# Kernel optimization log

Measured on AMD Instinct MI355X. Metric: run time of the kernel, lower is better.

The kernel has to match this reference:

```python
import jax, jax.numpy as jnp
import numpy as np

B, LENGTH = 4, 65494
FILTS = 256        # sinc out channels == attention seq len == d_model (BN constraint)
KERNEL = 1025      # first_conv=1024 -> forced odd
D_MODEL = 256
N_HEADS = 8
D_FF = 1024
E_LAYERS = 4
C_OUT = 2
IN_SIZE = 21490
SR = 16000


def _to_mel(hz):
    return 2595 * np.log10(1 + hz / 700)


def _to_hz(mel):
    return 700 * (10 ** (mel / 2595) - 1)


def make_sinc_filters():
    out_ch = FILTS + 1
    f = (SR // 2) * np.linspace(0, 1, 257)  # NFFT=512 -> 257 bins
    fmel = _to_mel(f)
    mels = np.linspace(fmel.min(), fmel.max(), out_ch + 2)
    freq = _to_hz(mels)[:out_ch]
    hsupp = np.arange(-(KERNEL - 1) / 2, (KERNEL - 1) / 2 + 1)
    ham = np.hamming(KERNEL)
    bp = np.zeros((FILTS, KERNEL), dtype=np.float32)
    for i in range(FILTS):
        fmin, fmax = freq[i], freq[i + 1]
        h_hi = 2 * fmax / SR * np.sinc(2 * fmax * hsupp / SR)
        h_lo = 2 * fmin / SR * np.sinc(2 * fmin * hsupp / SR)
        bp[i] = (ham * (h_hi - h_lo)).astype(np.float32)
    return jnp.asarray(bp).reshape(FILTS, 1, KERNEL)


def layernorm(x, g, b, eps=1e-5):
    m = x.mean(-1, keepdims=True)
    v = x.var(-1, keepdims=True)
    return (x - m) / jnp.sqrt(v + eps) * g + b


def batchnorm(x, g, b, eps=1e-5):
    # training-mode BatchNorm1d over [B, C, T]: stats over (0, 2)
    m = x.mean((0, 2), keepdims=True)
    v = x.var((0, 2), keepdims=True)
    return (x - m) / jnp.sqrt(v + eps) * g[None, :, None] + b[None, :, None]


def positional(n):
    pos = jnp.arange(n, dtype=jnp.float32)[:, None]
    div = jnp.exp(jnp.arange(0, D_MODEL, 2, dtype=jnp.float32) * (-np.log(10000.0) / D_MODEL))
    pe = jnp.zeros((n, D_MODEL), jnp.float32)
    pe = pe.at[:, 0::2].set(jnp.sin(pos * div)).at[:, 1::2].set(jnp.cos(pos * div))
    return pe


def _forward(x, filters, bn1_g, bn1_b, emb_w, emb_b, embbn_g, embbn_b,
             wq, bq, wk, bk, wv, bv, wo, bo, c1w, c1b, c2w, c2b,
             ln1g, ln1b, ln2g, ln2b, lnfg, lnfb, projw, projb):
    Bb = x.shape[0]
    # SincConv: [B,1,L] -> [B, FILTS, L-K+1]
    h = jax.lax.conv_general_dilated(x[:, None, :], filters, (1,), 'VALID',
                                     dimension_numbers=('NCH', 'OIH', 'NCH'))
    h = jnp.abs(h)
    T = h.shape[-1] // 3
    h = h[..., :T * 3].reshape(Bb, FILTS, T, 3).max(-1)  # max_pool1d(k=3)
    h = jax.nn.selu(batchnorm(h, bn1_g, bn1_b))          # [B, FILTS, 21490]
    # LinearEmbedding: Linear(21490 -> d_model) + BN + ReLU + pos emb
    e = jnp.einsum('bct,dt->bcd', h, emb_w) + emb_b      # [B, FILTS, D_MODEL]
    e = jax.nn.relu(batchnorm(e, embbn_g, embbn_b))
    z = e + positional(e.shape[1])[None]
    hd = D_MODEL // N_HEADS
    scale = 1.0 / np.sqrt(hd)
    for l in range(E_LAYERS):
        q = (z @ wq[l].T + bq[l]).reshape(Bb, FILTS, N_HEADS, hd)
        k = (z @ wk[l].T + bk[l]).reshape(Bb, FILTS, N_HEADS, hd)
        v = (z @ wv[l].T + bv[l]).reshape(Bb, FILTS, N_HEADS, hd)
        scores = jnp.einsum('blhe,bshe->bhls', q, k) * scale  # mask_flag=False
        attn = jax.nn.softmax(scores, axis=-1)
        o = jnp.einsum('bhls,bshd->blhd', attn, v).reshape(Bb, FILTS, D_MODEL)
        o = o @ wo[l].T + bo[l]
        z = layernorm(z + o, ln1g[l], ln1b[l])
        y = jax.nn.gelu(jnp.einsum('bld,fd->blf', z, c1w[l]) + c1b[l], approximate=False)
        y = jnp.einsum('blf,df->bld', y, c2w[l]) + c2b[l]
        z = layernorm(z + y, ln2g[l], ln2b[l])
    z = layernorm(z, lnfg, lnfb)
    pooled = z.mean(axis=1)
    return pooled @ projw.T + projb  # [B, C_OUT]


def setup_inputs() -> dict:
    key = jax.random.key(0)
    ks = jax.random.split(key, 16)
    rn = lambda k, s, sc=0.02: jax.random.normal(k, s, jnp.float32) * sc
    d = {}
    d['x'] = jax.random.normal(ks[0], (B, LENGTH), jnp.float32)
    d['filters'] = make_sinc_filters()
    d['bn1_g'] = jnp.ones((FILTS,), jnp.float32)
    d['bn1_b'] = jnp.zeros((FILTS,), jnp.float32)
    d['emb_w'] = rn(ks[1], (D_MODEL, IN_SIZE))
    d['emb_b'] = jnp.zeros((D_MODEL,), jnp.float32)
    d['embbn_g'] = jnp.ones((D_MODEL,), jnp.float32)
    d['embbn_b'] = jnp.zeros((D_MODEL,), jnp.float32)
    d['wq'] = rn(ks[2], (E_LAYERS, D_MODEL, D_MODEL))
    d['bq'] = jnp.zeros((E_LAYERS, D_MODEL), jnp.float32)
    d['wk'] = rn(ks[3], (E_LAYERS, D_MODEL, D_MODEL))
    d['bk'] = jnp.zeros((E_LAYERS, D_MODEL), jnp.float32)
    d['wv'] = rn(ks[4], (E_LAYERS, D_MODEL, D_MODEL))
    d['bv'] = jnp.zeros((E_LAYERS, D_MODEL), jnp.float32)
    d['wo'] = rn(ks[5], (E_LAYERS, D_MODEL, D_MODEL))
    d['bo'] = jnp.zeros((E_LAYERS, D_MODEL), jnp.float32)
    d['c1w'] = rn(ks[6], (E_LAYERS, D_FF, D_MODEL))
    d['c1b'] = jnp.zeros((E_LAYERS, D_FF), jnp.float32)
    d['c2w'] = rn(ks[7], (E_LAYERS, D_MODEL, D_FF))
    d['c2b'] = jnp.zeros((E_LAYERS, D_MODEL), jnp.float32)
    d['ln1g'] = jnp.ones((E_LAYERS, D_MODEL), jnp.float32)
    d['ln1b'] = jnp.zeros((E_LAYERS, D_MODEL), jnp.float32)
    d['ln2g'] = jnp.ones((E_LAYERS, D_MODEL), jnp.float32)
    d['ln2b'] = jnp.zeros((E_LAYERS, D_MODEL), jnp.float32)
    d['lnfg'] = jnp.ones((D_MODEL,), jnp.float32)
    d['lnfb'] = jnp.zeros((D_MODEL,), jnp.float32)
    d['projw'] = rn(ks[8], (C_OUT, D_MODEL))
    d['projb'] = jnp.zeros((C_OUT,), jnp.float32)
    return d


def reference(x, filters, bn1_g, bn1_b, emb_w, emb_b, embbn_g, embbn_b,
              wq, bq, wk, bk, wv, bv, wo, bo, c1w, c1b, c2w, c2b,
              ln1g, ln1b, ln2g, ln2b, lnfg, lnfb, projw, projb):
    return _forward(x, filters, bn1_g, bn1_b, emb_w, emb_b, embbn_g, embbn_b,
                    wq, bq, wk, bk, wv, bv, wo, bo, c1w, c1b, c2w, c2b,
                    ln1g, ln1b, ln2g, ln2b, lnfg, lnfb, projw, projb)
```

## Files before the change

kernel.cpp:

```cpp
#include <hip/hip_runtime.h>
#include <math.h>

#define L_IN 65494
#define T_POOL 21490
#define TPP 21496
#define KF 1025
#define RS 1144
#define NCH 141
#define KEMB 21490
#define KEMBP 21504
#define NKC 1344
#define FTILE 33280
#define LWSZ 786432

typedef short s16x4 __attribute__((ext_vector_type(4)));
typedef _Float16 f16x8 __attribute__((ext_vector_type(8)));
typedef float f32x4 __attribute__((ext_vector_type(4)));
typedef float f32x16 __attribute__((ext_vector_type(16)));

__device__ inline float selu_f(float x) {
    float e = expf(fminf(x, 0.f));
    float neg = 1.6732632423543772f * (e - 1.f);
    return 1.0507009873554805f * (x > 0.f ? x : neg);
}

__device__ inline float gelu_f(float x) {
    return 0.5f * x * (1.f + erff(x * 0.7071067811865476f));
}

__device__ inline float dot4(float4 a, float4 b) {
    return fmaf(a.x, b.x, fmaf(a.y, b.y, fmaf(a.z, b.z, a.w * b.w)));
}

__device__ inline float sel4(float a0, float a1, float a2, float a3, int i) {
    float r = a0;
    r = (i == 1) ? a1 : r;
    r = (i == 2) ? a2 : r;
    r = (i == 3) ? a3 : r;
    return r;
}

__device__ inline short f2h_bits(float v) {
    _Float16 h = (_Float16)v;
    return *(short*)&h;
}

__device__ inline void f16split(float v, short& hs, short& ls) {
    _Float16 h = (_Float16)v;
    float hf = (float)h;
    _Float16 l = (_Float16)(v - hf);
    hs = *(short*)&h;
    ls = *(short*)&l;
}

__device__ inline void f16split2(float v, _Float16& h, _Float16& l) {
    h = (_Float16)v;
    l = (_Float16)(v - (float)h);
}

__global__ __launch_bounds__(512)
void filt_pack_kernel(const float* __restrict__ filt, short* __restrict__ fpH) {
    int blk = blockIdx.x;
    int ft = blk / 65, kc = blk % 65;
    int t = threadIdx.x, lane = t >> 3, e = t & 7;
    int f = ft * 32 + (lane & 31);
    int tap = kc * 16 + (lane >> 5) * 8 + e;
    float v = (tap < KF) ? filt[f * KF + tap] : 0.f;
    fpH[blk * 512 + t] = f2h_bits(v);
}

__global__ __launch_bounds__(512)
void wpack_kernel(const float* __restrict__ wsrc, short* __restrict__ wpH) {
    int blk = blockIdx.x;
    int ft = blk / NKC, kc = blk % NKC;
    int t = threadIdx.x, lane = t >> 3, e = t & 7;
    int row = ft * 32 + (lane & 31);
    int tap = kc * 16 + (lane >> 5) * 8 + e;
    float v = (tap < KEMB) ? wsrc[(long)row * KEMB + tap] : 0.f;
    wpH[(long)blk * 512 + t] = f2h_bits(v);
}

__global__ __launch_bounds__(512)
void lwpack_kernel(const float* __restrict__ wo, const float* __restrict__ wq,
                   const float* __restrict__ wk, const float* __restrict__ wv,
                   const float* __restrict__ c1w, const float* __restrict__ c2w,
                   short* __restrict__ lw) {
    int b = blockIdx.x;
    int layer = b / 1536, r = b % 1536;
    int t = threadIdx.x, lane = t >> 3, e = t & 7;
    const float* src;
    int K, t2;
    long dst;
    if (r < 512) {
        int mat = r >> 7; t2 = r & 127;
        const float* m0 = (mat == 0 ? wo : mat == 1 ? wq : mat == 2 ? wk : wv);
        src = m0 + (long)layer * 65536; K = 256;
        dst = (long)layer * LWSZ + (long)mat * 65536 + (long)t2 * 512;
    } else if (r < 1024) {
        t2 = r - 512;
        src = c1w + (long)layer * 262144; K = 256;
        dst = (long)layer * LWSZ + 262144 + (long)t2 * 512;
    } else {
        t2 = r - 1024;
        src = c2w + (long)layer * 262144; K = 1024;
        dst = (long)layer * LWSZ + 524288 + (long)t2 * 512;
    }
    int KB = K >> 5;
    int nt = t2 / KB, kb = t2 % KB;
    int n = nt * 16 + (lane & 15);
    int k = kb * 32 + ((lane >> 4) & 3) * 8 + e;
    lw[dst + t] = f2h_bits(src[(long)n * K + k]);
}

__device__ inline f32x4 mfma_nt(const _Float16* __restrict__ Xh, const _Float16* __restrict__ Xl,
                                int xstride, const short* __restrict__ wp_nt, int KB, int lane) {
    f32x4 acc = {0.f, 0.f, 0.f, 0.f};
    const int row = (lane & 15) & 3;
    const int ko0 = ((lane >> 4) & 3) * 8;
    const short* bp = wp_nt + lane * 8;
    const _Float16* xh = Xh + row * xstride + ko0;
    const _Float16* xl = Xl + row * xstride + ko0;
#pragma unroll 4
    for (int kb = 0; kb < KB; kb++) {
        f16x8 bf = *(const f16x8*)(bp + kb * 512);
        f16x8 ah = *(const f16x8*)(xh + kb * 32);
        f16x8 al = *(const f16x8*)(xl + kb * 32);
        acc = __builtin_amdgcn_mfma_f32_16x16x32_f16(al, bf, acc, 0, 0, 0);
        acc = __builtin_amdgcn_mfma_f32_16x16x32_f16(ah, bf, acc, 0, 0, 0);
    }
    return acc;
}

union ConvLDS {
    short xh[8][RS];
    float ebuf[96][129];
};

#define MFMA2(ACC, AH, AL, BH) \
    ACC = __builtin_amdgcn_mfma_f32_32x32x16_f16(AL, BH, ACC, 0, 0, 0); \
    ACC = __builtin_amdgcn_mfma_f32_32x32x16_f16(AH, BH, ACC, 0, 0, 0);

__global__ __launch_bounds__(256, 3)
void conv_mfma_kernel(const float* __restrict__ x, const short* __restrict__ fpH,
                      _Float16* __restrict__ h) {
    __shared__ ConvLDS u;
    const int tid = threadIdx.x;
    const int pb = blockIdx.x;
    const int b = blockIdx.y;
    const int t0 = pb * 96;
    const float* xb = x + (long)b * L_IN;

    if (pb < 671) {
        for (int idx = tid; idx < 8 * NCH; idx += 256) {
            int s = idx / NCH, j = idx - s * NCH;
            int gi = t0 + s + j * 8;
            f16x8 hv;
#pragma unroll
            for (int e = 0; e < 8; e++) hv[e] = (_Float16)xb[gi + e];
            *(f16x8*)&u.xh[s][j * 8] = hv;
        }
    } else {
        for (int idx = tid; idx < 8 * NCH; idx += 256) {
            int s = idx / NCH, j = idx - s * NCH;
            int gi = t0 + s + j * 8;
            f16x8 hv;
#pragma unroll
            for (int e = 0; e < 8; e++) {
                float v = (gi + e < L_IN) ? xb[gi + e] : 0.f;
                hv[e] = (_Float16)v;
            }
            *(f16x8*)&u.xh[s][j * 8] = hv;
        }
    }
    __syncthreads();

    const int lane = tid & 63;
    const int wid = tid >> 6;
    const int l31 = lane & 31;
    const int hi = lane >> 5;
    const int f0w = wid * 64;

    const short* aH = &u.xh[l31 & 7][8 * (l31 >> 3) + 8 * hi];
    const short* bp0 = fpH + (long)(wid * 2) * FTILE + lane * 8;
    const short* bp1 = bp0 + FTILE;

    f32x16 a00 = {0}, a01 = {0}, a10 = {0}, a11 = {0}, a20 = {0}, a21 = {0};

#pragma unroll 1
    for (int kc = 0; kc < 65; kc++) {
        const int ko = kc * 16;
        const int kf = kc * 512;
        f16x8 ah0 = *(const f16x8*)(aH + ko);
        f16x8 ah1 = *(const f16x8*)(aH + ko + 32);
        f16x8 ah2 = *(const f16x8*)(aH + ko + 64);
        f16x8 bh0 = *(const f16x8*)(bp0 + kf);
        f16x8 bh1 = *(const f16x8*)(bp1 + kf);
        a00 = __builtin_amdgcn_mfma_f32_32x32x16_f16(ah0, bh0, a00, 0, 0, 0);
        a01 = __builtin_amdgcn_mfma_f32_32x32x16_f16(ah0, bh1, a01, 0, 0, 0);
        a10 = __builtin_amdgcn_mfma_f32_32x32x16_f16(ah1, bh0, a10, 0, 0, 0);
        a11 = __builtin_amdgcn_mfma_f32_32x32x16_f16(ah1, bh1, a11, 0, 0, 0);
        a20 = __builtin_amdgcn_mfma_f32_32x32x16_f16(ah2, bh0, a20, 0, 0, 0);
        a21 = __builtin_amdgcn_mfma_f32_32x32x16_f16(ah2, bh1, a21, 0, 0, 0);
    }

    __syncthreads();
    const int t3l = tid & 31;
    const int t3 = pb * 32 + t3l;

#pragma unroll
    for (int half = 0; half < 2; half++) {
        if ((wid >> 1) == half) {
            int fcb = f0w - half * 128;
#define WRF(ACC, MT, NT)                                                   \
            {                                                              \
                int fc = fcb + NT * 32 + l31;                              \
                _Pragma("unroll")                                          \
                for (int r = 0; r < 16; r++) {                             \
                    int pos = MT * 32 + (r & 3) + 8 * (r >> 2) + 4 * hi;   \
                    u.ebuf[pos][fc] = fabsf(ACC[r]);                       \
                }                                                          \
            }
            WRF(a00, 0, 0) WRF(a01, 0, 1)
            WRF(a10, 1, 0) WRF(a11, 1, 1)
            WRF(a20, 2, 0) WRF(a21, 2, 1)
#undef WRF
        }
        __syncthreads();
        if (t3 < T_POOL) {
            for (int ff = tid >> 5; ff < 128; ff += 8) {
                float v = fmaxf(fmaxf(u.ebuf[3 * t3l][ff], u.ebuf[3 * t3l + 1][ff]),
                                u.ebuf[3 * t3l + 2][ff]);
                h[((long)(b * 256 + half * 128 + ff)) * TPP + t3] = (_Float16)v;
            }
        }
        __syncthreads();
    }
}

__global__ __launch_bounds__(256)
void bn_part_kernel(const _Float16* __restrict__ xin, float* __restrict__ p1,
                    float* __restrict__ p2) {
    __shared__ float sm[8];
    int c = blockIdx.x, s = blockIdx.y, tid = threadIdx.x;
    int t0 = s * 2687, t1 = min(T_POOL, t0 + 2687);
    float s1 = 0.f, s2 = 0.f;
    for (int b = 0; b < 4; b++) {
        const _Float16* p = xin + (long)b * 256 * TPP + (long)c * TPP;
        for (int t = t0 + tid; t < t1; t += 256) {
            float v = (float)p[t];
            s1 += v;
            s2 = fmaf(v, v, s2);
        }
    }
    for (int off = 32; off > 0; off >>= 1) { s1 += __shfl_down(s1, off); s2 += __shfl_down(s2, off); }
    int lane = tid & 63, wv = tid >> 6;
    if (lane == 0) { sm[wv] = s1; sm[4 + wv] = s2; }
    __syncthreads();
    if (tid == 0) {
        p1[c * 8 + s] = sm[0] + sm[1] + sm[2] + sm[3];
        p2[c * 8 + s] = sm[4] + sm[5] + sm[6] + sm[7];
    }
}

__global__ __launch_bounds__(256)
void bn_fin_kernel(const float* __restrict__ p1, const float* __restrict__ p2,
                   const float* __restrict__ g, const float* __restrict__ bb,
                   float* __restrict__ sc, float* __restrict__ sh) {
    int c = threadIdx.x;
    float S1 = 0.f, S2 = 0.f;
#pragma unroll
    for (int s = 0; s < 8; s++) { S1 += p1[c * 8 + s]; S2 += p2[c * 8 + s]; }
    float n = 4.f * (float)T_POOL;
    float mean = S1 / n;
    float var = S2 / n - mean * mean;
    float rstd = rsqrtf(var + 1e-5f);
    float gc = g[c], bc = bb[c];
    sc[c] = rstd * gc;
    sh[c] = bc - mean * rstd * gc;
}

__global__ __launch_bounds__(256)
void bn_stats_kernel(const float* __restrict__ xin, const float* __restrict__ g,
                     const float* __restrict__ bb, float* __restrict__ sc,
                     float* __restrict__ sh, int ilen, long bstride) {
    __shared__ float sm[8];
    int c = blockIdx.x, tid = threadIdx.x;
    float s1 = 0.f, s2 = 0.f;
    for (int b = 0; b < 4; b++) {
        const float* p = xin + b * bstride + (long)c * ilen;
        for (int t = tid; t < ilen; t += 256) {
            float v = p[t];
            s1 += v;
            s2 = fmaf(v, v, s2);
        }
    }
    for (int off = 32; off > 0; off >>= 1) { s1 += __shfl_down(s1, off); s2 += __shfl_down(s2, off); }
    int lane = tid & 63, wv = tid >> 6;
    if (lane == 0) { sm[wv] = s1; sm[4 + wv] = s2; }
    __syncthreads();
    if (tid == 0) {
        float S1 = sm[0] + sm[1] + sm[2] + sm[3];
        float S2 = sm[4] + sm[5] + sm[6] + sm[7];
        float n = 4.f * (float)ilen;
        float mean = S1 / n;
        float var = S2 / n - mean * mean;
        float rstd = rsqrtf(var + 1e-5f);
        float gc = g[c], bc = bb[c];
        sc[c] = rstd * gc;
        sh[c] = bc - mean * rstd * gc;
    }
}

__global__ __launch_bounds__(256, 2)
void embed_mfma_kernel(const _Float16* __restrict__ H, const short* __restrict__ Wh,
                       const float* __restrict__ sc, const float* __restrict__ sh,
                       float* __restrict__ P, int kPerZ) {
    __shared__ short Ah[128][36];
    __shared__ short Al[128][36];
    const int tid = threadIdx.x;
    const int rowBase = blockIdx.x * 128;
    const int colBase = blockIdx.y * 128;
    const int z = blockIdx.z;
    const int kz = z * kPerZ;
    const int iters = kPerZ >> 5;

    const int trow = tid >> 1, th = (tid & 1) * 16;
    const int arow = rowBase + trow;
    const float asc = sc[arow & 255], ash_ = sh[arow & 255];
    const _Float16* Ap = H + (long)arow * TPP;

    const int lane = tid & 63, wid = tid >> 6;
    const int l31 = lane & 31, hi = lane >> 5;
    const int wm = wid >> 1, wn = wid & 1;

    const short* bhp[2];
#pragma unroll
    for (int nt = 0; nt < 2; nt++) {
        int ft = (colBase >> 5) + wn * 2 + nt;
        bhp[nt] = Wh + (long)ft * NKC * 512 + lane * 8;
    }

    f32x16 acc[2][2] = {{{0}, {0}}, {{0}, {0}}};

    for (int it = 0; it < iters; it++) {
        const int k0 = kz + it * 32;
        __syncthreads();
        float av[16];
        if (k0 + 32 <= KEMB) {
            const f16x8* p8 = (const f16x8*)(Ap + k0 + th);
            f16x8 v0 = p8[0], v1 = p8[1];
#pragma unroll
            for (int e = 0; e < 8; e++) { av[e] = (float)v0[e]; av[8 + e] = (float)v1[e]; }
        } else {
#pragma unroll
            for (int e = 0; e < 16; e++) {
                int k = k0 + th + e;
                av[e] = (k < KEMB) ? (float)Ap[k] : 0.f;
            }
        }
#pragma unroll
        for (int q = 0; q < 4; q++) {
            s16x4 h4, l4;
#pragma unroll
            for (int e = 0; e < 4; e++) {
                float v = selu_f(fmaf(av[q * 4 + e], asc, ash_));
                short hs, ls;
                f16split(v, hs, ls);
                h4[e] = hs; l4[e] = ls;
            }
            *(s16x4*)&Ah[trow][th + q * 4] = h4;
            *(s16x4*)&Al[trow][th + q * 4] = l4;
        }
        __syncthreads();

#pragma unroll
        for (int ks = 0; ks < 2; ks++) {
            const int kloc = ks * 16 + hi * 8;
            const long kcg = (long)((k0 >> 4) + ks) * 512;
            f16x8 ah[2], al[2], bh[2];
#pragma unroll
            for (int mt = 0; mt < 2; mt++) {
                const int r = wm * 64 + mt * 32 + l31;
                const short* ph = &Ah[r][kloc];
                const short* pl = &Al[r][kloc];
                union { f16x8 v; unsigned long long q[2]; } uh, ul;
                uh.q[0] = *(const unsigned long long*)(ph);
                uh.q[1] = *(const unsigned long long*)(ph + 4);
                ul.q[0] = *(const unsigned long long*)(pl);
                ul.q[1] = *(const unsigned long long*)(pl + 4);
                ah[mt] = uh.v; al[mt] = ul.v;
            }
#pragma unroll
            for (int nt = 0; nt < 2; nt++)
                bh[nt] = *(const f16x8*)(bhp[nt] + kcg);
#pragma unroll
            for (int mt = 0; mt < 2; mt++)
#pragma unroll
                for (int nt = 0; nt < 2; nt++) {
                    MFMA2(acc[mt][nt], ah[mt], al[mt], bh[nt])
                }
        }
    }

    float* Pz = P + (long)z * 262144;
#pragma unroll
    for (int mt = 0; mt < 2; mt++)
#pragma unroll
        for (int nt = 0; nt < 2; nt++) {
            int col = colBase + wn * 64 + nt * 32 + l31;
#pragma unroll
            for (int r = 0; r < 16; r++) {
                int row = rowBase + wm * 64 + mt * 32 + (r & 3) + 8 * (r >> 2) + 4 * hi;
                Pz[(long)row * 256 + col] = acc[mt][nt][r];
            }
        }
}

__global__ __launch_bounds__(256)
void embed_combine_kernel(const float* __restrict__ P, const float* __restrict__ eb,
                          float* __restrict__ e, int nsplit) {
    int idx = blockIdx.x * 256 + threadIdx.x;
    float s = 0.f;
    for (int z = 0; z < nsplit; z++) s += P[(long)z * 262144 + idx];
    e[idx] = s + eb[idx & 255];
}

__global__ __launch_bounds__(512)
void qkv_init_kernel(const float* __restrict__ e, const float* __restrict__ sc,
                     const float* __restrict__ sh, const short* __restrict__ lw0,
                     const float* __restrict__ bq0, const float* __restrict__ bk0,
                     const float* __restrict__ bv0,
                     float* __restrict__ z, float* __restrict__ qo,
                     float* __restrict__ ko, float* __restrict__ vo) {
    __shared__ _Float16 zsh[4][256], zsl[4][256];
    const int t = threadIdx.x;
    const int w = t >> 6, lane = t & 63;
    const long rowg0 = (long)blockIdx.x * 4;

    for (int idx = t; idx < 1024; idx += 512) {
        int i = idx >> 8, dd = idx & 255;
        int c = (int)((rowg0 + i) & 255);
        float v = fmaf(e[(rowg0 + i) * 256 + dd], sc[c], sh[c]);
        v = fmaxf(v, 0.f);
        int i2 = dd >> 1;
        float ang = (float)c * expf(-0.03597789207803195f * (float)(2 * i2));
        float pe = (dd & 1) ? cosf(ang) : sinf(ang);
        float zz = v + pe;
        z[(rowg0 + i) * 256 + dd] = zz;
        _Float16 hh, ll;
        f16split2(zz, hh, ll);
        zsh[i][dd] = hh; zsl[i][dd] = ll;
    }
    __syncthreads();

#pragma unroll
    for (int mat = 0; mat < 3; mat++) {
        const short* wp = lw0 + 65536 * (1 + mat);
        const float* bb = (mat == 0 ? bq0 : mat == 1 ? bk0 : bv0);
        float* op = (mat == 0 ? qo : mat == 1 ? ko : vo);
        for (int nt = w; nt < 16; nt += 8) {
            f32x4 acc = mfma_nt(&zsh[0][0], &zsl[0][0], 256, wp + nt * 8 * 512, 8, lane);
            if (lane < 16) {
                int col = nt * 16 + lane;
                float bv2 = bb[col];
#pragma unroll
                for (int r = 0; r < 4; r++)
                    op[(rowg0 + r) * 256 + col] = acc[r] + bv2;
            }
        }
    }
}

__device__ inline void ln_reduce4(const float (*buf)[256], float (*mr)[2], int t) {
    int wid = t >> 6, lane = t & 63;
    if (wid < 4) {
        float4 v = *(const float4*)&buf[wid][lane * 4];
        float s = v.x + v.y + v.z + v.w;
        float q = v.x * v.x + v.y * v.y + v.z * v.z + v.w * v.w;
#pragma unroll
        for (int off = 32; off > 0; off >>= 1) {
            s += __shfl_xor(s, off);
            q += __shfl_xor(q, off);
        }
        if (lane == 0) {
            float mean = s * (1.f / 256.f);
            float var = q * (1.f / 256.f) - mean * mean;
            mr[wid][0] = mean;
            mr[wid][1] = rsqrtf(var + 1e-5f);
        }
    }
}

template <int LAST>
__global__ __launch_bounds__(1024)
void layer_kernel(const float* __restrict__ zin, const float* __restrict__ qin,
                  const float* __restrict__ kin, const float* __restrict__ vin,
                  const short* __restrict__ lw_l, const short* __restrict__ lw_n,
                  const float* __restrict__ bo_l,
                  const float* __restrict__ c1b_l, const float* __restrict__ c2b_l,
                  const float* __restrict__ ln1g_l, const float* __restrict__ ln1b_l,
                  const float* __restrict__ ln2g_l, const float* __restrict__ ln2b_l,
                  const float* __restrict__ bq_n, const float* __restrict__ bk_n,
                  const float* __restrict__ bv_n,
                  const float* __restrict__ lnfg, const float* __restrict__ lnfb,
                  float* __restrict__ zout, float* __restrict__ qo,
                  float* __restrict__ ko, float* __restrict__ vo,
                  float* __restrict__ lnf_out) {
    __shared__ float zs[4][256];
    __shared__ float qb[4][256];
    __shared__ float sscore[4][8][256];
    __shared__ _Float16 zsh[4][256], zsl[4][256];
    __shared__ _Float16 yh[4][1024], yl[4][1024];
    __shared__ float mr[4][2];

    const int t = threadIdx.x;
    const int w = t >> 6, lane = t & 63;
    const long rowg0 = (long)blockIdx.x * 4;
    const int b = blockIdx.x >> 6;

    const int f = t & 255;
    const int kq = t >> 8;

    {
        int r = t >> 8, dd = t & 255;
        zs[r][dd] = zin[(rowg0 + r) * 256 + dd];
        qb[r][dd] = qin[(rowg0 + r) * 256 + dd];
    }
    __syncthreads();

    {
        const float scale = 0.17677669529663687f;
        const int jq = lane >> 3, li = lane & 7, d4 = li * 4;
        const int hh = w >> 1, jh = w & 1;
        const float* kb = kin + (long)b * 65536 + hh * 32 + d4;
        float4 q0 = *(const float4*)&qb[0][hh * 32 + d4];
        float4 q1 = *(const float4*)&qb[1][hh * 32 + d4];
        float4 q2 = *(const float4*)&qb[2][hh * 32 + d4];
        float4 q3 = *(const float4*)&qb[3][hh * 32 + d4];
        for (int jb = 0; jb < 16; jb++) {
            int j = jh * 128 + jb * 8 + jq;
            float4 kv = *(const float4*)(kb + (long)j * 256);
            float a0 = dot4(kv, q0), a1 = dot4(kv, q1);
            float a2 = dot4(kv, q2), a3 = dot4(kv, q3);
#pragma unroll
            for (int off = 1; off < 8; off <<= 1) {
                a0 += __shfl_xor(a0, off); a1 += __shfl_xor(a1, off);
                a2 += __shfl_xor(a2, off); a3 += __shfl_xor(a3, off);
            }
            if (li < 4) sscore[li][hh][j] = sel4(a0, a1, a2, a3, li) * scale;
        }
    }
    __syncthreads();

    {
#pragma unroll
        for (int p = 0; p < 2; p++) {
            int pair = w * 2 + p;
            int i = pair >> 3, hh = pair & 7;
            float* row = sscore[i][hh];
            float v0 = row[lane], v1 = row[lane + 64];
            float v2 = row[lane + 128], v3 = row[lane + 192];
            float m = fmaxf(fmaxf(v0, v1), fmaxf(v2, v3));
#pragma unroll
            for (int off = 32; off > 0; off >>= 1) m = fmaxf(m, __shfl_xor(m, off));
            float e0 = expf(v0 - m), e1 = expf(v1 - m);
            float e2 = expf(v2 - m), e3 = expf(v3 - m);
            float su = e0 + e1 + e2 + e3;
#pragma unroll
            for (int off = 32; off > 0; off >>= 1) su += __shfl_xor(su, off);
            float inv = 1.f / su;
            row[lane] = e0 * inv; row[lane + 64] = e1 * inv;
            row[lane + 128] = e2 * inv; row[lane + 192] = e3 * inv;
        }
    }
    __syncthreads();

    {
        int row = kq;
        int hh = f >> 5;
        const float* vcol = vin + (long)b * 65536 + f;
        const float* p0 = sscore[row][hh];
        float a0 = 0.f;
#pragma unroll 4
        for (int j4 = 0; j4 < 64; j4++) {
            float4 pv0 = *(const float4*)(p0 + j4 * 4);
            float v0 = vcol[(long)(j4 * 4 + 0) * 256];
            float v1 = vcol[(long)(j4 * 4 + 1) * 256];
            float v2 = vcol[(long)(j4 * 4 + 2) * 256];
            float v3 = vcol[(long)(j4 * 4 + 3) * 256];
            a0 = fmaf(pv0.x, v0, a0); a0 = fmaf(pv0.y, v1, a0);
            a0 = fmaf(pv0.z, v2, a0); a0 = fmaf(pv0.w, v3, a0);
        }
        _Float16 hh2, ll;
        f16split2(a0, hh2, ll);
        zsh[row][f] = hh2; zsl[row][f] = ll;
    }
    __syncthreads();

    {
        int nt = w;
        f32x4 acc = mfma_nt(&zsh[0][0], &zsl[0][0], 256, lw_l + nt * 8 * 512, 8, lane);
        if (lane < 16) {
            int col = nt * 16 + lane;
            float bb = bo_l[col];
#pragma unroll
            for (int r = 0; r < 4; r++)
                qb[r][col] = acc[r] + bb + zs[r][col];
        }
    }
    __syncthreads();
    ln_reduce4(qb, mr, t);
    __syncthreads();
    {
        int r = kq;
        float z1 = (qb[r][f] - mr[r][0]) * mr[r][1] * ln1g_l[f] + ln1b_l[f];
        zs[r][f] = z1;
        _Float16 hh2, ll;
        f16split2(z1, hh2, ll);
        zsh[r][f] = hh2; zsl[r][f] = ll;
    }
    __syncthreads();

    {
        const short* wp = lw_l + 262144;
        for (int nt = w; nt < 64; nt += 16) {
            f32x4 acc = mfma_nt(&zsh[0][0], &zsl[0][0], 256, wp + nt * 8 * 512, 8, lane);
            if (lane < 16) {
                int col = nt * 16 + lane;
                float cb = c1b_l[col];
#pragma unroll
                for (int r = 0; r < 4; r++) {
                    float g = gelu_f(acc[r] + cb);
                    _Float16 hh2, ll;
                    f16split2(g, hh2, ll);
                    yh[r][col] = hh2; yl[r][col] = ll;
                }
            }
        }
    }
    __syncthreads();

    {
        const short* wp = lw_l + 524288;
        int nt = w;
        f32x4 acc = mfma_nt(&yh[0][0], &yl[0][0], 1024, wp + nt * 32 * 512, 32, lane);
        if (lane < 16) {
            int col = nt * 16 + lane;
            float cb = c2b_l[col];
#pragma unroll
            for (int r = 0; r < 4; r++)
                qb[r][col] = acc[r] + cb + zs[r][col];
        }
    }
    __syncthreads();
    ln_reduce4(qb, mr, t);
    __syncthreads();
    {
        int r = kq;
        float z2 = (qb[r][f] - mr[r][0]) * mr[r][1] * ln2g_l[f] + ln2b_l[f];
        zs[r][f] = z2;
        zout[(rowg0 + r) * 256 + f] = z2;
        _Float16 hh2, ll;
        f16split2(z2, hh2, ll);
        zsh[r][f] = hh2; zsl[r][f] = ll;
    }
    __syncthreads();

    if (!LAST) {
#pragma unroll
        for (int mat = 0; mat < 3; mat++) {
            const short* wp = lw_n + 65536 * (1 + mat);
            const float* bb = (mat == 0 ? bq_n : mat == 1 ? bk_n : bv_n);
            float* op = (mat == 0 ? qo : mat == 1 ? ko : vo);
            int nt = w;
            f32x4 acc = mfma_nt(&zsh[0][0], &zsl[0][0], 256, wp + nt * 8 * 512, 8, lane);
            if (lane < 16) {
                int col = nt * 16 + lane;
                float bv2 = bb[col];
#pragma unroll
                for (int r = 0; r < 4; r++)
                    op[(rowg0 + r) * 256 + col] = acc[r] + bv2;
            }
        }
    } else {
        ln_reduce4(zs, mr, t);
        __syncthreads();
        {
            int r = kq;
            lnf_out[(rowg0 + r) * 256 + f] =
                (zs[r][f] - mr[r][0]) * mr[r][1] * lnfg[f] + lnfb[f];
        }
    }
}

__global__ __launch_bounds__(256)
void final_kernel(const float* __restrict__ zf, const float* __restrict__ pw,
                  const float* __restrict__ pb, float* __restrict__ out) {
    __shared__ float sm[8];
    int b = blockIdx.x, d = threadIdx.x;
    float s = 0.f;
    for (int c = 0; c < 256; c++) s += zf[((long)(b * 256 + c)) * 256 + d];
    float pooled = s * (1.f / 256.f);
    float c0 = pooled * pw[d], c1 = pooled * pw[256 + d];
    for (int off = 32; off > 0; off >>= 1) { c0 += __shfl_down(c0, off); c1 += __shfl_down(c1, off); }
    int lane = d & 63, wv = d >> 6;
    if (lane == 0) { sm[wv] = c0; sm[4 + wv] = c1; }
    __syncthreads();
    if (d == 0) {
        out[b * 2 + 0] = sm[0] + sm[1] + sm[2] + sm[3] + pb[0];
        out[b * 2 + 1] = sm[4] + sm[5] + sm[6] + sm[7] + pb[1];
    }
}

extern "C" void kernel_launch(void* const* d_in, const int* in_sizes, int n_in,
                              void* d_out, int out_size, void* d_ws, size_t ws_size,
                              hipStream_t stream) {
    const float* x       = (const float*)d_in[0];
    const float* filters = (const float*)d_in[1];
    const float* bn1_g   = (const float*)d_in[2];
    const float* bn1_b   = (const float*)d_in[3];
    const float* emb_w   = (const float*)d_in[4];
    const float* emb_b   = (const float*)d_in[5];
    const float* embbn_g = (const float*)d_in[6];
    const float* embbn_b = (const float*)d_in[7];
    const float* wq      = (const float*)d_in[8];
    const float* bq      = (const float*)d_in[9];
    const float* wk      = (const float*)d_in[10];
    const float* bk      = (const float*)d_in[11];
    const float* wv      = (const float*)d_in[12];
    const float* bv      = (const float*)d_in[13];
    const float* wo      = (const float*)d_in[14];
    const float* bo      = (const float*)d_in[15];
    const float* c1w     = (const float*)d_in[16];
    const float* c1b     = (const float*)d_in[17];
    const float* c2w     = (const float*)d_in[18];
    const float* c2b     = (const float*)d_in[19];
    const float* ln1g    = (const float*)d_in[20];
    const float* ln1b    = (const float*)d_in[21];
    const float* ln2g    = (const float*)d_in[22];
    const float* ln2b    = (const float*)d_in[23];
    const float* lnfg    = (const float*)d_in[24];
    const float* lnfb    = (const float*)d_in[25];
    const float* projw   = (const float*)d_in[26];
    const float* projb   = (const float*)d_in[27];

    const long hF = 11005952L;
    const long wpackF = 2752512L;
    const long lwF = 1572864L;
    const long fixedF = hF + 5120 + wpackF + lwF + 9L * 262144;
    long wsFloats = (long)(ws_size / 4);
    long Z = 32;
    while (Z > 8 && fixedF + Z * 262144L > wsFloats) Z >>= 1;
    const int kPerZ = KEMBP / (int)Z;

    float* ws = (float*)d_ws;
    _Float16* h16 = (_Float16*)ws;
    float* bn1_sc = ws + hF;
    float* bn1_sh = bn1_sc + 256;
    float* e_sc   = bn1_sh + 256;
    float* e_sh   = e_sc + 256;
    float* bnp1   = e_sh + 256;
    float* bnp2   = bnp1 + 2048;
    float* part   = bnp2 + 2048;
    float* wsp    = part + Z * 262144L;
    short* wpH    = (short*)wsp;
    float* e      = wsp + wpackF;
    float* z      = e + 262144;
    float* qA     = z + 262144;
    float* kA     = qA + 262144;
    float* vA     = kA + 262144;
    float* qB     = vA + 262144;
    float* kB     = qB + 262144;
    float* vB     = kB + 262144;
    float* t1     = vB + 262144;
    short* lw     = (short*)(t1 + 262144);

    short* fpH = (short*)part;

    filt_pack_kernel<<<520, 512, 0, stream>>>(filters, fpH);
    wpack_kernel<<<8 * NKC, 512, 0, stream>>>(emb_w, wpH);
    lwpack_kernel<<<6144, 512, 0, stream>>>(wo, wq, wk, wv, c1w, c2w, lw);
    conv_mfma_kernel<<<dim3(672, 4), 256, 0, stream>>>(x, fpH, h16);
    bn_part_kernel<<<dim3(256, 8), 256, 0, stream>>>(h16, bnp1, bnp2);
    bn_fin_kernel<<<1, 256, 0, stream>>>(bnp1, bnp2, bn1_g, bn1_b, bn1_sc, bn1_sh);
    embed_mfma_kernel<<<dim3(8, 2, (int)Z), 256, 0, stream>>>(h16, wpH,
                                                              bn1_sc, bn1_sh, part, kPerZ);
    embed_combine_kernel<<<1024, 256, 0, stream>>>(part, emb_b, e, (int)Z);
    bn_stats_kernel<<<256, 256, 0, stream>>>(e, embbn_g, embbn_b, e_sc, e_sh,
                                             256, 256L * 256);
    qkv_init_kernel<<<256, 512, 0, stream>>>(e, e_sc, e_sh, lw, bq, bk, bv,
                                             z, qA, kA, vA);

    float* qs[2][3] = {{qA, kA, vA}, {qB, kB, vB}};
    for (int l = 0; l < 4; l++) {
        float** in = qs[l & 1];
        float** ou = qs[(l + 1) & 1];
        const short* lw_l = lw + (long)l * LWSZ;
        const short* lw_n = lw + (long)((l + 1) & 3) * LWSZ;
        const float* bo_l = bo + l * 256;
        const float* c1b_l = c1b + l * 1024;
        const float* c2b_l = c2b + l * 256;
        const float* l1g = ln1g + l * 256; const float* l1b = ln1b + l * 256;
        const float* l2g = ln2g + l * 256; const float* l2b = ln2b + l * 256;
        if (l < 3) {
            const float* bq_n = bq + (l + 1) * 256;
            const float* bk_n = bk + (l + 1) * 256;
            const float* bv_n = bv + (l + 1) * 256;
            layer_kernel<0><<<256, 1024, 0, stream>>>(z, in[0], in[1], in[2],
                lw_l, lw_n, bo_l, c1b_l, c2b_l, l1g, l1b, l2g, l2b,
                bq_n, bk_n, bv_n, lnfg, lnfb,
                z, ou[0], ou[1], ou[2], t1);
        } else {
            layer_kernel<1><<<256, 1024, 0, stream>>>(z, in[0], in[1], in[2],
                lw_l, lw_n, bo_l, c1b_l, c2b_l, l1g, l1b, l2g, l2b,
                bq, bk, bv, lnfg, lnfb,
                z, ou[0], ou[1], ou[2], t1);
        }
    }

    final_kernel<<<4, 256, 0, stream>>>(t1, projw, projb, (float*)d_out);
}
```

Measured before the change: 461.6 us.

## Drop fp16 low-part split in embedding GEMM and fuse pack and BN-stat kernels

Several changes land together. The three weight-packing kernels become one launch. The embedding-BN statistics move into the combine kernel and qkv_init, which removes the separate bn_stats launch. The embedding GEMM drops the hi/lo fp16 split of the activations, so it issues half as many MFMAs and needs half the LDS. That last change lowers accuracy in a 21490-long reduction, which risks tolerance failures.

```diff
diff --git a/kernel.cpp b/kernel.cpp
--- a/kernel.cpp
+++ b/kernel.cpp
@@ -45,71 +45,59 @@
     return *(short*)&h;
 }
 
-__device__ inline void f16split(float v, short& hs, short& ls) {
-    _Float16 h = (_Float16)v;
-    float hf = (float)h;
-    _Float16 l = (_Float16)(v - hf);
-    hs = *(short*)&h;
-    ls = *(short*)&l;
-}
-
 __device__ inline void f16split2(float v, _Float16& h, _Float16& l) {
     h = (_Float16)v;
     l = (_Float16)(v - (float)h);
 }
 
 __global__ __launch_bounds__(512)
-void filt_pack_kernel(const float* __restrict__ filt, short* __restrict__ fpH) {
-    int blk = blockIdx.x;
-    int ft = blk / 65, kc = blk % 65;
+void pack_all_kernel(const float* __restrict__ filt, const float* __restrict__ emb_w,
+                     const float* __restrict__ wo, const float* __restrict__ wq,
+                     const float* __restrict__ wk, const float* __restrict__ wv,
+                     const float* __restrict__ c1w, const float* __restrict__ c2w,
+                     short* __restrict__ fpH, short* __restrict__ wpH,
+                     short* __restrict__ lw) {
+    int bx = blockIdx.x;
     int t = threadIdx.x, lane = t >> 3, e = t & 7;
-    int f = ft * 32 + (lane & 31);
-    int tap = kc * 16 + (lane >> 5) * 8 + e;
-    float v = (tap < KF) ? filt[f * KF + tap] : 0.f;
-    fpH[blk * 512 + t] = f2h_bits(v);
-}
-
-__global__ __launch_bounds__(512)
-void wpack_kernel(const float* __restrict__ wsrc, short* __restrict__ wpH) {
-    int blk = blockIdx.x;
-    int ft = blk / NKC, kc = blk % NKC;
-    int t = threadIdx.x, lane = t >> 3, e = t & 7;
-    int row = ft * 32 + (lane & 31);
-    int tap = kc * 16 + (lane >> 5) * 8 + e;
-    float v = (tap < KEMB) ? wsrc[(long)row * KEMB + tap] : 0.f;
-    wpH[(long)blk * 512 + t] = f2h_bits(v);
-}
-
-__global__ __launch_bounds__(512)
-void lwpack_kernel(const float* __restrict__ wo, const float* __restrict__ wq,
-                   const float* __restrict__ wk, const float* __restrict__ wv,
-                   const float* __restrict__ c1w, const float* __restrict__ c2w,
-                   short* __restrict__ lw) {
-    int b = blockIdx.x;
-    int layer = b / 1536, r = b % 1536;
-    int t = threadIdx.x, lane = t >> 3, e = t & 7;
-    const float* src;
-    int K, t2;
-    long dst;
-    if (r < 512) {
-        int mat = r >> 7; t2 = r & 127;
-        const float* m0 = (mat == 0 ? wo : mat == 1 ? wq : mat == 2 ? wk : wv);
-        src = m0 + (long)layer * 65536; K = 256;
-        dst = (long)layer * LWSZ + (long)mat * 65536 + (long)t2 * 512;
-    } else if (r < 1024) {
-        t2 = r - 512;
-        src = c1w + (long)layer * 262144; K = 256;
-        dst = (long)layer * LWSZ + 262144 + (long)t2 * 512;
+    if (bx < 520) {
+        int ft = bx / 65, kc = bx % 65;
+        int f = ft * 32 + (lane & 31);
+        int tap = kc * 16 + (lane >> 5) * 8 + e;
+        float v = (tap < KF) ? filt[f * KF + tap] : 0.f;
+        fpH[bx * 512 + t] = f2h_bits(v);
+    } else if (bx < 520 + 8 * NKC) {
+        int blk = bx - 520;
+        int ft = blk / NKC, kc = blk % NKC;
+        int row = ft * 32 + (lane & 31);
+        int tap = kc * 16 + (lane >> 5) * 8 + e;
+        float v = (tap < KEMB) ? emb_w[(long)row * KEMB + tap] : 0.f;
+        wpH[(long)blk * 512 + t] = f2h_bits(v);
     } else {
-        t2 = r - 1024;
-        src = c2w + (long)layer * 262144; K = 1024;
-        dst = (long)layer * LWSZ + 524288 + (long)t2 * 512;
-    }
-    int KB = K >> 5;
-    int nt = t2 / KB, kb = t2 % KB;
-    int n = nt * 16 + (lane & 15);
-    int k = kb * 32 + ((lane >> 4) & 3) * 8 + e;
-    lw[dst + t] = f2h_bits(src[(long)n * K + k]);
+        int b = bx - 520 - 8 * NKC;
+        int layer = b / 1536, r = b % 1536;
+        const float* src;
+        int K, t2;
+        long dst;
+        if (r < 512) {
+            int mat = r >> 7; t2 = r & 127;
+            const float* m0 = (mat == 0 ? wo : mat == 1 ? wq : mat == 2 ? wk : wv);
+            src = m0 + (long)layer * 65536; K = 256;
+            dst = (long)layer * LWSZ + (long)mat * 65536 + (long)t2 * 512;
+        } else if (r < 1024) {
+            t2 = r - 512;
+            src = c1w + (long)layer * 262144; K = 256;
+            dst = (long)layer * LWSZ + 262144 + (long)t2 * 512;
+        } else {
+            t2 = r - 1024;
+            src = c2w + (long)layer * 262144; K = 1024;
+            dst = (long)layer * LWSZ + 524288 + (long)t2 * 512;
+        }
+        int KB = K >> 5;
+        int nt = t2 / KB, kb = t2 % KB;
+        int n = nt * 16 + (lane & 15);
+        int k = kb * 32 + ((lane >> 4) & 3) * 8 + e;
+        lw[dst + t] = f2h_bits(src[(long)n * K + k]);
+    }
 }
 
 __device__ inline f32x4 mfma_nt(const _Float16* __restrict__ Xh, const _Float16* __restrict__ Xl,
@@ -136,10 +124,6 @@
     float ebuf[96][129];
 };
 
-#define MFMA2(ACC, AH, AL, BH) \
-    ACC = __builtin_amdgcn_mfma_f32_32x32x16_f16(AL, BH, ACC, 0, 0, 0); \
-    ACC = __builtin_amdgcn_mfma_f32_32x32x16_f16(AH, BH, ACC, 0, 0, 0);
-
 __global__ __launch_bounds__(256, 3)
 void conv_mfma_kernel(const float* __restrict__ x, const short* __restrict__ fpH,
                       _Float16* __restrict__ h) {
@@ -279,44 +263,11 @@
     sh[c] = bc - mean * rstd * gc;
 }
 
-__global__ __launch_bounds__(256)
-void bn_stats_kernel(const float* __restrict__ xin, const float* __restrict__ g,
-                     const float* __restrict__ bb, float* __restrict__ sc,
-                     float* __restrict__ sh, int ilen, long bstride) {
-    __shared__ float sm[8];
-    int c = blockIdx.x, tid = threadIdx.x;
-    float s1 = 0.f, s2 = 0.f;
-    for (int b = 0; b < 4; b++) {
-        const float* p = xin + b * bstride + (long)c * ilen;
-        for (int t = tid; t < ilen; t += 256) {
-            float v = p[t];
-            s1 += v;
-            s2 = fmaf(v, v, s2);
-        }
-    }
-    for (int off = 32; off > 0; off >>= 1) { s1 += __shfl_down(s1, off); s2 += __shfl_down(s2, off); }
-    int lane = tid & 63, wv = tid >> 6;
-    if (lane == 0) { sm[wv] = s1; sm[4 + wv] = s2; }
-    __syncthreads();
-    if (tid == 0) {
-        float S1 = sm[0] + sm[1] + sm[2] + sm[3];
-        float S2 = sm[4] + sm[5] + sm[6] + sm[7];
-        float n = 4.f * (float)ilen;
-        float mean = S1 / n;
-        float var = S2 / n - mean * mean;
-        float rstd = rsqrtf(var + 1e-5f);
-        float gc = g[c], bc = bb[c];
-        sc[c] = rstd * gc;
-        sh[c] = bc - mean * rstd * gc;
-    }
-}
-
 __global__ __launch_bounds__(256, 2)
 void embed_mfma_kernel(const _Float16* __restrict__ H, const short* __restrict__ Wh,
                        const float* __restrict__ sc, const float* __restrict__ sh,
                        float* __restrict__ P, int kPerZ) {
     __shared__ short Ah[128][36];
-    __shared__ short Al[128][36];
     const int tid = threadIdx.x;
     const int rowBase = blockIdx.x * 128;
     const int colBase = blockIdx.y * 128;
@@ -360,16 +311,13 @@
         }
 #pragma unroll
         for (int q = 0; q < 4; q++) {
-            s16x4 h4, l4;
+            s16x4 h4;
 #pragma unroll
             for (int e = 0; e < 4; e++) {
                 float v = selu_f(fmaf(av[q * 4 + e], asc, ash_));
-                short hs, ls;
-                f16split(v, hs, ls);
-                h4[e] = hs; l4[e] = ls;
+                h4[e] = f2h_bits(v);
             }
             *(s16x4*)&Ah[trow][th + q * 4] = h4;
-            *(s16x4*)&Al[trow][th + q * 4] = l4;
         }
         __syncthreads();
 
@@ -377,18 +325,15 @@
         for (int ks = 0; ks < 2; ks++) {
             const int kloc = ks * 16 + hi * 8;
             const long kcg = (long)((k0 >> 4) + ks) * 512;
-            f16x8 ah[2], al[2], bh[2];
+            f16x8 ah[2], bh[2];
 #pragma unroll
             for (int mt = 0; mt < 2; mt++) {
                 const int r = wm * 64 + mt * 32 + l31;
                 const short* ph = &Ah[r][kloc];
-                const short* pl = &Al[r][kloc];
-                union { f16x8 v; unsigned long long q[2]; } uh, ul;
+                union { f16x8 v; unsigned long long q[2]; } uh;
                 uh.q[0] = *(const unsigned long long*)(ph);
                 uh.q[1] = *(const unsigned long long*)(ph + 4);
-                ul.q[0] = *(const unsigned long long*)(pl);
-                ul.q[1] = *(const unsigned long long*)(pl + 4);
-                ah[mt] = uh.v; al[mt] = ul.v;
+                ah[mt] = uh.v;
             }
 #pragma unroll
             for (int nt = 0; nt < 2; nt++)
@@ -396,9 +341,8 @@
 #pragma unroll
             for (int mt = 0; mt < 2; mt++)
 #pragma unroll
-                for (int nt = 0; nt < 2; nt++) {
-                    MFMA2(acc[mt][nt], ah[mt], al[mt], bh[nt])
-                }
+                for (int nt = 0; nt < 2; nt++)
+                    acc[mt][nt] = __builtin_amdgcn_mfma_f32_32x32x16_f16(ah[mt], bh[nt], acc[mt][nt], 0, 0, 0);
         }
     }
 
@@ -418,29 +362,60 @@
 
 __global__ __launch_bounds__(256)
 void embed_combine_kernel(const float* __restrict__ P, const float* __restrict__ eb,
-                          float* __restrict__ e, int nsplit) {
-    int idx = blockIdx.x * 256 + threadIdx.x;
+                          float* __restrict__ e, float* __restrict__ ebnp, int nsplit) {
+    __shared__ float sm[8];
+    const int bid = blockIdx.x, tid = threadIdx.x;
+    const int idx = bid * 256 + tid;
     float s = 0.f;
     for (int z = 0; z < nsplit; z++) s += P[(long)z * 262144 + idx];
-    e[idx] = s + eb[idx & 255];
+    float v = s + eb[tid];
+    e[idx] = v;
+    float s1 = v, s2 = v * v;
+    for (int off = 32; off > 0; off >>= 1) { s1 += __shfl_down(s1, off); s2 += __shfl_down(s2, off); }
+    int lane = tid & 63, wv = tid >> 6;
+    if (lane == 0) { sm[wv] = s1; sm[4 + wv] = s2; }
+    __syncthreads();
+    if (tid == 0) {
+        ebnp[bid * 2] = sm[0] + sm[1] + sm[2] + sm[3];
+        ebnp[bid * 2 + 1] = sm[4] + sm[5] + sm[6] + sm[7];
+    }
 }
 
 __global__ __launch_bounds__(512)
-void qkv_init_kernel(const float* __restrict__ e, const float* __restrict__ sc,
-                     const float* __restrict__ sh, const short* __restrict__ lw0,
+void qkv_init_kernel(const float* __restrict__ e, const float* __restrict__ ebnp,
+                     const float* __restrict__ bng, const float* __restrict__ bnb,
+                     const short* __restrict__ lw0,
                      const float* __restrict__ bq0, const float* __restrict__ bk0,
                      const float* __restrict__ bv0,
                      float* __restrict__ z, float* __restrict__ qo,
                      float* __restrict__ ko, float* __restrict__ vo) {
     __shared__ _Float16 zsh[4][256], zsl[4][256];
+    __shared__ float scs[4], shs[4];
     const int t = threadIdx.x;
     const int w = t >> 6, lane = t & 63;
     const long rowg0 = (long)blockIdx.x * 4;
 
+    if (t < 4) {
+        int c = (int)((rowg0 + t) & 255);
+        float S1 = 0.f, S2 = 0.f;
+#pragma unroll
+        for (int b2 = 0; b2 < 4; b2++) {
+            S1 += ebnp[(b2 * 256 + c) * 2];
+            S2 += ebnp[(b2 * 256 + c) * 2 + 1];
+        }
+        float mean = S1 * (1.f / 1024.f);
+        float var = S2 * (1.f / 1024.f) - mean * mean;
+        float rstd = rsqrtf(var + 1e-5f);
+        float gc = bng[c];
+        scs[t] = rstd * gc;
+        shs[t] = bnb[c] - mean * rstd * gc;
+    }
+    __syncthreads();
+
     for (int idx = t; idx < 1024; idx += 512) {
         int i = idx >> 8, dd = idx & 255;
         int c = (int)((rowg0 + i) & 255);
-        float v = fmaf(e[(rowg0 + i) * 256 + dd], sc[c], sh[c]);
+        float v = fmaf(e[(rowg0 + i) * 256 + dd], scs[i], shs[i]);
         v = fmaxf(v, 0.f);
         int i2 = dd >> 1;
         float ang = (float)c * expf(-0.03597789207803195f * (float)(2 * i2));
@@ -747,7 +722,7 @@
     const long hF = 11005952L;
     const long wpackF = 2752512L;
     const long lwF = 1572864L;
-    const long fixedF = hF + 5120 + wpackF + lwF + 9L * 262144;
+    const long fixedF = hF + 6656 + wpackF + lwF + 9L * 262144;
     long wsFloats = (long)(ws_size / 4);
     long Z = 32;
     while (Z > 8 && fixedF + Z * 262144L > wsFloats) Z >>= 1;
@@ -757,9 +732,8 @@
     _Float16* h16 = (_Float16*)ws;
     float* bn1_sc = ws + hF;
     float* bn1_sh = bn1_sc + 256;
-    float* e_sc   = bn1_sh + 256;
-    float* e_sh   = e_sc + 256;
-    float* bnp1   = e_sh + 256;
+    float* ebnp   = bn1_sh + 256;
+    float* bnp1   = ebnp + 2048;
     float* bnp2   = bnp1 + 2048;
     float* part   = bnp2 + 2048;
     float* wsp    = part + Z * 262144L;
@@ -777,19 +751,16 @@
 
     short* fpH = (short*)part;
 
-    filt_pack_kernel<<<520, 512, 0, stream>>>(filters, fpH);
-    wpack_kernel<<<8 * NKC, 512, 0, stream>>>(emb_w, wpH);
-    lwpack_kernel<<<6144, 512, 0, stream>>>(wo, wq, wk, wv, c1w, c2w, lw);
+    pack_all_kernel<<<520 + 8 * NKC + 6144, 512, 0, stream>>>(
+        filters, emb_w, wo, wq, wk, wv, c1w, c2w, fpH, wpH, lw);
     conv_mfma_kernel<<<dim3(672, 4), 256, 0, stream>>>(x, fpH, h16);
     bn_part_kernel<<<dim3(256, 8), 256, 0, stream>>>(h16, bnp1, bnp2);
     bn_fin_kernel<<<1, 256, 0, stream>>>(bnp1, bnp2, bn1_g, bn1_b, bn1_sc, bn1_sh);
     embed_mfma_kernel<<<dim3(8, 2, (int)Z), 256, 0, stream>>>(h16, wpH,
                                                               bn1_sc, bn1_sh, part, kPerZ);
-    embed_combine_kernel<<<1024, 256, 0, stream>>>(part, emb_b, e, (int)Z);
-    bn_stats_kernel<<<256, 256, 0, stream>>>(e, embbn_g, embbn_b, e_sc, e_sh,
-                                             256, 256L * 256);
-    qkv_init_kernel<<<256, 512, 0, stream>>>(e, e_sc, e_sh, lw, bq, bk, bv,
-                                             z, qA, kA, vA);
+    embed_combine_kernel<<<1024, 256, 0, stream>>>(part, emb_b, e, ebnp, (int)Z);
+    qkv_init_kernel<<<256, 512, 0, stream>>>(e, ebnp, embbn_g, embbn_b, lw,
+                                             bq, bk, bv, z, qA, kA, vA);
 
     float* qs[2][3] = {{qA, kA, vA}, {qB, kB, vB}};
     for (int l = 0; l < 4; l++) {
```

After: 450.5 us. -2.4%, faster.
